# Kernel optimization log

Measured on AMD Instinct MI355X. Metric: run time of the kernel, lower is better.

## Reference

```python
import jax, jax.numpy as jnp
import numpy as np

B, N_NODE, E_PER, C, HID, HEADS, IN, NL = 16, 1024, 8192, 16, 128, 4, 32, 2
N = B * N_NODE
NEG_SLOPE = 0.2


def setup_inputs() -> dict:
    key = jax.random.key(0)
    ks = jax.random.split(key, 16)
    obs = jax.random.normal(ks[0], (N, IN), jnp.float32)
    # per-graph random edges, guaranteed no self-loops (GATv2Conv re-adds them once)
    src_l = jax.random.randint(ks[1], (B, E_PER), 0, N_NODE)
    off = jax.random.randint(ks[2], (B, E_PER), 1, N_NODE)
    dst_l = (src_l + off) % N_NODE
    base = (jnp.arange(B) * N_NODE)[:, None]
    edge_index = jnp.stack([(src_l + base).reshape(-1), (dst_l + base).reshape(-1)]).astype(jnp.int32)

    def lin(k, fi, fo):
        return (jax.random.normal(k, (fi, fo), jnp.float32) / np.sqrt(fi)).astype(jnp.float32)

    def gat(k):
        sk = jax.random.split(k, 3)
        return {
            'Wl': (jax.random.normal(sk[0], (NL, HID, HEADS * HID), jnp.float32) / np.sqrt(HID)),
            'bl': jnp.zeros((NL, HEADS * HID), jnp.float32),
            'Wr': (jax.random.normal(sk[1], (NL, HID, HEADS * HID), jnp.float32) / np.sqrt(HID)),
            'br': jnp.zeros((NL, HEADS * HID), jnp.float32),
            'att': (jax.random.normal(sk[2], (NL, HEADS, HID), jnp.float32) / np.sqrt(HID)),
            'bias': jnp.zeros((NL, HID), jnp.float32),
            'g': jnp.ones((NL, HID), jnp.float32),
            'beta': jnp.zeros((NL, HID), jnp.float32),
        }

    inp = {'obs': obs, 'edge_index': edge_index, 'n_node': N_NODE,
           'emb_W': lin(ks[3], IN, HID), 'emb_b': jnp.zeros((HID,), jnp.float32),
           'pool_W': lin(ks[4], HID, C), 'pool_b': jnp.zeros((C,), jnp.float32),
           'mlp_W1': lin(ks[5], HID, 4 * HID), 'mlp_b1': jnp.zeros((4 * HID,), jnp.float32),
           'mlp_W2': lin(ks[6], 4 * HID, HID), 'mlp_b2': jnp.zeros((HID,), jnp.float32)}
    for nm, d in (('low', gat(ks[7])), ('high', gat(ks[8]))):
        for k2, v in d.items():
            inp[nm + '_' + k2] = v
    return inp


def _layer_norm(x, g, b):
    mu = x.mean(-1, keepdims=True)
    v = jnp.mean((x - mu) ** 2, -1, keepdims=True)
    return (x - mu) / jnp.sqrt(v + 1e-5) * g + b


def _gatv2(x, src, dst, Wl, bl, Wr, br, att, bias):
    # GATv2Conv: heads H, concat=False (mean over heads), eval mode (no dropout)
    n = x.shape[0]
    H, D = att.shape
    xl = (x @ Wl + bl).reshape(n, H, D)  # source transform (lin_l)
    xr = (x @ Wr + br).reshape(n, H, D)  # target transform (lin_r)
    e = jax.nn.leaky_relu(xl[src] + xr[dst], NEG_SLOPE)  # [E,H,D]
    logit = jnp.einsum('ehd,hd->eh', e, att)
    m = jax.ops.segment_max(logit, dst, num_segments=n)
    p = jnp.exp(logit - m[dst])
    z = jax.ops.segment_sum(p, dst, num_segments=n)
    alpha = p / z[dst]
    out = jax.ops.segment_sum(alpha[:, :, None] * xl[src], dst, num_segments=n)
    return out.mean(axis=1) + bias


def _gat_stack(h, src, dst, Wl, bl, Wr, br, att, bias, g, beta):
    h_res = h
    nl = Wl.shape[0]
    for j in range(nl):
        h_in = h
        h = _gatv2(h, src, dst, Wl[j], bl[j], Wr[j], br[j], att[j], bias[j])
        h = _layer_norm(h, g[j], beta[j])
        if j != nl - 1:
            h = jax.nn.silu(h)
        h = h + h_in  # use_res=True
    return h + h_res


def _forward(obs, edge_index, n_node, emb_W, emb_b, pool_W, pool_b, mlp_W1, mlp_b1, mlp_W2, mlp_b2,
             low_Wl, low_bl, low_Wr, low_br, low_att, low_bias, low_g, low_beta,
             high_Wl, high_bl, high_Wr, high_br, high_att, high_bias, high_g, high_beta):
    n = obs.shape[0]
    h = obs @ emb_W + emb_b
    hh = h
    # low-level edges + self-loops (GATv2Conv add_self_loops; input has none)
    loops = jnp.arange(n, dtype=edge_index.dtype)
    src = jnp.concatenate([edge_index[0], loops])
    dst = jnp.concatenate([edge_index[1], loops])
    h = _gat_stack(h, src, dst, low_Wl, low_bl, low_Wr, low_br, low_att, low_bias, low_g, low_beta)
    # soft pooling
    pooling = jax.nn.softmax(h @ pool_W + pool_b, axis=-1)  # dim=1 == last dim on 2D
    b = n // n_node
    c = pooling.shape[-1]
    s = pooling.reshape(b, n_node, c)
    count = jnp.maximum(s.sum(axis=1), 1e-5)  # sT @ ones, clamp_min(1e-5)
    Hf = jnp.einsum('bnc,bnd->bcd', s, h.reshape(b, n_node, -1)) / count[:, :, None]
    Hf = Hf.reshape(b * c, -1)
    # high-level: fully connected per-graph cluster edges (self-loops already present once)
    hr = jnp.repeat(jnp.arange(c, dtype=jnp.int32), c)
    hc = jnp.tile(jnp.arange(c, dtype=jnp.int32), c)
    offb = (jnp.arange(b, dtype=jnp.int32) * c)[:, None]
    hsrc = (hr[None, :] + offb).reshape(-1)
    hdst = (hc[None, :] + offb).reshape(-1)
    Hf = _gat_stack(Hf, hsrc, hdst, high_Wl, high_bl, high_Wr, high_br, high_att, high_bias, high_g, high_beta)
    # unpool + residual MLP (BaseMLP flat=True: hidden=4*HID, Tanh, residual)
    l_H = jnp.einsum('bnc,bcd->bnd', s, Hf.reshape(b, c, -1)).reshape(n, -1)
    x = l_H + hh
    return jnp.tanh(x @ mlp_W1 + mlp_b1) @ mlp_W2 + mlp_b2 + x


def reference(obs, edge_index, n_node, emb_W, emb_b, pool_W, pool_b, mlp_W1, mlp_b1, mlp_W2, mlp_b2,
              low_Wl, low_bl, low_Wr, low_br, low_att, low_bias, low_g, low_beta,
              high_Wl, high_bl, high_Wr, high_br, high_att, high_bias, high_g, high_beta):
    return _forward(obs, edge_index, n_node, emb_W, emb_b, pool_W, pool_b, mlp_W1, mlp_b1, mlp_W2, mlp_b2,
                    low_Wl, low_bl, low_Wr, low_br, low_att, low_bias, low_g, low_beta,
                    high_Wl, high_bl, high_Wr, high_br, high_att, high_bias, high_g, high_beta)
```

## Files before the change

kernel.cpp:

```cpp
#include <hip/hip_runtime.h>
#include <math.h>

#define NTOT  16384
#define NNODE 1024

typedef unsigned short u16;
typedef unsigned short u16x8 __attribute__((ext_vector_type(8)));
typedef short s16x8 __attribute__((ext_vector_type(8)));
typedef float f32x4 __attribute__((ext_vector_type(4)));

static __device__ __forceinline__ float b2f(u16 u) {
  return __uint_as_float(((unsigned)u) << 16);
}
static __device__ __forceinline__ u16 f2b(float f) {
  unsigned x = __float_as_uint(f);
  return (u16)((x + 0x7FFFu + ((x >> 16) & 1u)) >> 16);
}

__global__ __launch_bounds__(64) void emb_k(const float* __restrict__ obs,
    const float* __restrict__ W, const float* __restrict__ b,
    float* __restrict__ h, float* __restrict__ hh, u16* __restrict__ h_bf)
{
  int n = blockIdx.x, l = threadIdx.x;
  __shared__ float ob[32];
  if (l < 32) ob[l] = obs[n * 32 + l];
  __syncthreads();
  float a0 = b[l], a1 = b[64 + l];
  #pragma unroll
  for (int k = 0; k < 32; ++k) {
    float o = ob[k];
    a0 = fmaf(o, W[k * 128 + l], a0);
    a1 = fmaf(o, W[k * 128 + 64 + l], a1);
  }
  size_t base = (size_t)n * 128;
  h[base + l] = a0;  h[base + 64 + l] = a1;
  hh[base + l] = a0; hh[base + 64 + l] = a1;
  h_bf[base + l] = f2b(a0); h_bf[base + 64 + l] = f2b(a1);
}

__global__ void hist_k(const int* __restrict__ ei, int E0, int* __restrict__ deg)
{
  int i = blockIdx.x * blockDim.x + threadIdx.x;
  int ET = E0 + NTOT;
  if (i < ET) {
    int d = (i < E0) ? ei[E0 + i] : (i - E0);
    atomicAdd(&deg[d], 1);
  }
}

__global__ __launch_bounds__(256) void scan_k(const int* __restrict__ deg,
    int* __restrict__ off, int* __restrict__ cursor)
{
  __shared__ int part[256];
  int t = threadIdx.x;
  int base = t * 64;
  int sum = 0;
  for (int i = 0; i < 64; ++i) sum += deg[base + i];
  part[t] = sum;
  __syncthreads();
  if (t == 0) {
    int run = 0;
    for (int i = 0; i < 256; ++i) { int v = part[i]; part[i] = run; run += v; }
  }
  __syncthreads();
  int run = part[t];
  for (int i = 0; i < 64; ++i) {
    off[base + i] = run; cursor[base + i] = run;
    run += deg[base + i];
  }
  if (t == 255) off[NTOT] = run;
}

__global__ void scat_k(const int* __restrict__ ei, int E0,
    int* __restrict__ cursor, int* __restrict__ csr_src)
{
  int i = blockIdx.x * blockDim.x + threadIdx.x;
  int ET = E0 + NTOT;
  if (i < ET) {
    int s, d;
    if (i < E0) { s = ei[i]; d = ei[E0 + i]; } else { s = d = i - E0; }
    int pos = atomicAdd(&cursor[d], 1);
    csr_src[pos] = s;
  }
}

__global__ void hi_k(int* __restrict__ hi_off, int* __restrict__ hi_src)
{
  int t = threadIdx.x;
  hi_off[t] = t * 16;
  if (t == 0) hi_off[256] = 4096;
  for (int i = t; i < 4096; i += 256) {
    int u = i >> 4;
    hi_src[i] = (u & ~15) + (i & 15);
  }
}

__global__ void wq_k(const float* __restrict__ W, u16* __restrict__ out,
                     int K, int N, int total)
{
  int idx = blockIdx.x * 256 + threadIdx.x;
  if (idx >= total) return;
  int kn = K * N;
  int m = idx / kn, r = idx - m * kn;
  int n = r / K, k = r - n * K;
  out[idx] = f2b(W[(size_t)m * kn + (size_t)k * N + n]);
}

__global__ __launch_bounds__(256) void gemm_bf16(
    const u16* __restrict__ A, const u16* __restrict__ Bt,
    const float* __restrict__ bias,
    float* __restrict__ Cf, u16* __restrict__ Cb,
    const float* __restrict__ res,
    int M, int K, int N, int act)
{
  __shared__ u16 Al[128][128];
  __shared__ u16 Bl[128][128];
  const int tid = threadIdx.x;
  const int bm = blockIdx.x * 128, bn = blockIdx.y * 128;
  const int w = tid >> 6, l = tid & 63;
  const int fr = l & 15;
  const int kg = l >> 4;
  const int sr = tid >> 1;
  const int sh = (tid & 1) << 3;

  f32x4 acc[2][8];
  #pragma unroll
  for (int a = 0; a < 2; ++a)
    #pragma unroll
    for (int b = 0; b < 8; ++b)
      acc[a][b] = (f32x4){0.f, 0.f, 0.f, 0.f};

  for (int k0 = 0; k0 < K; k0 += 128) {
    __syncthreads();
    const u16* As = A + (size_t)(bm + sr) * K + k0 + (sh << 3);
    const u16* Bs = Bt + (size_t)(bn + sr) * K + k0 + (sh << 3);
    #pragma unroll
    for (int i = 0; i < 8; ++i) {
      int gs = (sh + i) ^ (sr & 7);
      *(uint4*)&Al[sr][gs << 3] = *(const uint4*)(As + (i << 3));
    }
    #pragma unroll
    for (int i = 0; i < 8; ++i) {
      int gs = (sh + i) ^ (sr & 7);
      *(uint4*)&Bl[sr][gs << 3] = *(const uint4*)(Bs + (i << 3));
    }
    __syncthreads();
    #pragma unroll
    for (int ks = 0; ks < 4; ++ks) {
      const int g = (ks << 2) + kg;
      const int ar0 = w * 32 + fr, ar1 = ar0 + 16;
      s16x8 a0 = *(const s16x8*)&Al[ar0][(g ^ (ar0 & 7)) << 3];
      s16x8 a1 = *(const s16x8*)&Al[ar1][(g ^ (ar1 & 7)) << 3];
      #pragma unroll
      for (int nr = 0; nr < 8; ++nr) {
        const int br = nr * 16 + fr;
        s16x8 bb = *(const s16x8*)&Bl[br][(g ^ (br & 7)) << 3];
        acc[0][nr] = __builtin_amdgcn_mfma_f32_16x16x32_bf16(a0, bb, acc[0][nr], 0, 0, 0);
        acc[1][nr] = __builtin_amdgcn_mfma_f32_16x16x32_bf16(a1, bb, acc[1][nr], 0, 0, 0);
      }
    }
  }

  #pragma unroll
  for (int mr = 0; mr < 2; ++mr) {
    const int row0 = bm + w * 32 + mr * 16 + (kg << 2);
    #pragma unroll
    for (int nr = 0; nr < 8; ++nr) {
      const int col = bn + nr * 16 + fr;
      const float bb = bias[col];
      #pragma unroll
      for (int j = 0; j < 4; ++j) {
        float v = acc[mr][nr][j] + bb;
        if (act) v = tanhf(v);
        size_t o = (size_t)(row0 + j) * N + col;
        if (res) v += res[o];
        if (Cf) Cf[o] = v;
        if (Cb) Cb[o] = f2b(v);
      }
    }
  }
}

__global__ __launch_bounds__(64) void gat_agg(
    const u16* __restrict__ xl, const u16* __restrict__ xr,
    const int* __restrict__ off, const int* __restrict__ srcs,
    const float* __restrict__ att, const float* __restrict__ bias,
    const float* __restrict__ g, const float* __restrict__ beta,
    float* __restrict__ h, u16* __restrict__ h_bf,
    const float* __restrict__ res2, int do_silu, int swz)
{
  int b = blockIdx.x, l = threadIdx.x;
  int dst;
  if (swz) {
    int xcd = b & 7, i = b >> 3;
    dst = (((xcd << 1) + (i >> 10)) << 10) | (i & 1023);
  } else dst = b;

  float xrr[8], attr[8];
  {
    u16x8 vx = *(const u16x8*)(xr + (size_t)dst * 512 + l * 8);
    #pragma unroll
    for (int i = 0; i < 8; ++i) xrr[i] = b2f(vx[i]);
    const float4 a0 = *(const float4*)(att + l * 8);
    const float4 a1 = *(const float4*)(att + l * 8 + 4);
    attr[0] = a0.x; attr[1] = a0.y; attr[2] = a0.z; attr[3] = a0.w;
    attr[4] = a1.x; attr[5] = a1.y; attr[6] = a1.z; attr[7] = a1.w;
  }
  int e0 = off[dst], e1 = off[dst + 1];
  float m = -1e30f, z = 0.f;
  float acc[8] = {0.f, 0.f, 0.f, 0.f, 0.f, 0.f, 0.f, 0.f};
  int sB = (e0 + 1 < e1) ? srcs[e0 + 1] : 0;
  u16x8 vcur = *(const u16x8*)(xl + (size_t)srcs[e0] * 512 + l * 8);
  for (int e = e0; e < e1; ++e) {
    u16x8 vv = vcur;
    if (e + 1 < e1) {
      vcur = *(const u16x8*)(xl + (size_t)sB * 512 + l * 8);
      if (e + 2 < e1) sB = srcs[e + 2];
    }
    float xv[8];
    #pragma unroll
    for (int i = 0; i < 8; ++i) xv[i] = b2f(vv[i]);
    float part = 0.f;
    #pragma unroll
    for (int i = 0; i < 8; ++i) {
      float v = xv[i] + xrr[i];
      v = v > 0.f ? v : 0.2f * v;
      part = fmaf(v, attr[i], part);
    }
    part += __shfl_xor(part, 1); part += __shfl_xor(part, 2);
    part += __shfl_xor(part, 4); part += __shfl_xor(part, 8);
    float mn = fmaxf(m, part);
    float sc = __expf(m - mn);
    float p = __expf(part - mn);
    z = z * sc + p;
    #pragma unroll
    for (int i = 0; i < 8; ++i) acc[i] = fmaf(acc[i], sc, p * xv[i]);
    m = mn;
  }
  float inv = 0.25f / z;
  int d0 = (l & 15) * 8;
  float o[8];
  #pragma unroll
  for (int i = 0; i < 8; ++i) {
    float v = acc[i] * inv;
    v += __shfl_xor(v, 16);
    v += __shfl_xor(v, 32);
    o[i] = v + bias[d0 + i];
  }
  float ssum = 0.f;
  #pragma unroll
  for (int i = 0; i < 8; ++i) ssum += o[i];
  ssum += __shfl_xor(ssum, 1); ssum += __shfl_xor(ssum, 2);
  ssum += __shfl_xor(ssum, 4); ssum += __shfl_xor(ssum, 8);
  float mu = ssum * (1.f / 128.f);
  float vs = 0.f;
  #pragma unroll
  for (int i = 0; i < 8; ++i) { float d = o[i] - mu; vs += d * d; }
  vs += __shfl_xor(vs, 1); vs += __shfl_xor(vs, 2);
  vs += __shfl_xor(vs, 4); vs += __shfl_xor(vs, 8);
  float rstd = rsqrtf(vs * (1.f / 128.f) + 1e-5f);
  if (l < 16) {
    size_t base = (size_t)dst * 128 + d0;
    float out[8];
    u16x8 hb;
    #pragma unroll
    for (int i = 0; i < 8; ++i) {
      float y = (o[i] - mu) * rstd * g[d0 + i] + beta[d0 + i];
      if (do_silu) y = y / (1.f + __expf(-y));
      float r = h[base + i];
      if (res2) r += res2[base + i];
      out[i] = y + r;
      hb[i] = f2b(out[i]);
    }
    *(float4*)(h + base) = make_float4(out[0], out[1], out[2], out[3]);
    *(float4*)(h + base + 4) = make_float4(out[4], out[5], out[6], out[7]);
    *(u16x8*)(h_bf + base) = hb;
  }
}

__global__ __launch_bounds__(256) void pool_k(const float* __restrict__ h,
    const float* __restrict__ W, const float* __restrict__ b, float* __restrict__ s)
{
  __shared__ float hs[16 * 130];
  __shared__ float Ws[128 * 16];
  int t = threadIdx.x;
  int n0 = blockIdx.x * 16;
  #pragma unroll
  for (int i = 0; i < 8; ++i) {
    int idx = t + 256 * i;
    hs[(idx >> 7) * 130 + (idx & 127)] = h[(size_t)n0 * 128 + idx];
    Ws[idx] = W[idx];
  }
  __syncthreads();
  int nl = t >> 4, c = t & 15;
  float acc = b[c];
  for (int k = 0; k < 128; ++k) acc = fmaf(hs[nl * 130 + k], Ws[k * 16 + c], acc);
  float mx = acc;
  mx = fmaxf(mx, __shfl_xor(mx, 1)); mx = fmaxf(mx, __shfl_xor(mx, 2));
  mx = fmaxf(mx, __shfl_xor(mx, 4)); mx = fmaxf(mx, __shfl_xor(mx, 8));
  float p = __expf(acc - mx), sum = p;
  sum += __shfl_xor(sum, 1); sum += __shfl_xor(sum, 2);
  sum += __shfl_xor(sum, 4); sum += __shfl_xor(sum, 8);
  s[(size_t)(n0 + nl) * 16 + c] = p / sum;
}

#define HF_CHUNK 32
#define HF_NCH   32
__global__ __launch_bounds__(256) void hfp_k(const float* __restrict__ s,
    const float* __restrict__ h, float* __restrict__ part, float* __restrict__ cpart)
{
  __shared__ float ss[HF_CHUNK][16];
  __shared__ float hs[HF_CHUNK][128];
  int b = blockIdx.x >> 5, chunk = blockIdx.x & 31;
  int n0 = b * NNODE + chunk * HF_CHUNK;
  int t = threadIdx.x;
  if (t < 128) {
    float4 v = *(const float4*)(s + (size_t)(n0 + (t >> 2)) * 16 + (t & 3) * 4);
    *(float4*)&ss[t >> 2][(t & 3) * 4] = v;
  }
  #pragma unroll
  for (int i = 0; i < 4; ++i) {
    int idx = t + 256 * i;
    int row = idx >> 5, c4 = (idx & 31) * 4;
    *(float4*)&hs[row][c4] = *(const float4*)(h + (size_t)(n0 + row) * 128 + c4);
  }
  __syncthreads();
  int d = t & 127, cg = (t >> 7) * 8;
  float acc[8] = {};
  for (int n = 0; n < HF_CHUNK; ++n) {
    float hv = hs[n][d];
    #pragma unroll
    for (int i = 0; i < 8; ++i) acc[i] = fmaf(ss[n][cg + i], hv, acc[i]);
  }
  float* po = part + (size_t)chunk * 32768 + (size_t)(b * 16 + cg) * 128 + d;
  #pragma unroll
  for (int i = 0; i < 8; ++i) po[i * 128] = acc[i];
  if (t < 16) {
    float c = 0.f;
    #pragma unroll
    for (int n = 0; n < HF_CHUNK; ++n) c += ss[n][t];
    cpart[chunk * 256 + b * 16 + t] = c;
  }
}

__global__ __launch_bounds__(256) void hfr_k(const float* __restrict__ part,
    const float* __restrict__ cpart, float* __restrict__ Hf,
    float* __restrict__ HfRes, u16* __restrict__ Hf_bf)
{
  int o = blockIdx.x * 256 + threadIdx.x;
  int bc = o >> 7;
  float a = 0.f, cnt = 0.f;
  #pragma unroll 8
  for (int ch = 0; ch < HF_NCH; ++ch) {
    a += part[(size_t)ch * 32768 + o];
    cnt += cpart[ch * 256 + bc];
  }
  float v = a / fmaxf(cnt, 1e-5f);
  Hf[o] = v; HfRes[o] = v; Hf_bf[o] = f2b(v);
}

__global__ __launch_bounds__(64) void unpool_k(const float* __restrict__ s,
    const float* __restrict__ Hf, const float* __restrict__ hh,
    float* __restrict__ x, u16* __restrict__ x_bf)
{
  int n = blockIdx.x, l = threadIdx.x;
  int b = n >> 10;
  float a0 = 0.f, a1 = 0.f;
  #pragma unroll
  for (int c = 0; c < 16; ++c) {
    float sv = s[(size_t)n * 16 + c];
    const float* hp = Hf + (size_t)((b << 4) + c) * 128;
    a0 = fmaf(sv, hp[l], a0);
    a1 = fmaf(sv, hp[64 + l], a1);
  }
  size_t base = (size_t)n * 128;
  float v0 = a0 + hh[base + l], v1 = a1 + hh[base + 64 + l];
  x[base + l] = v0; x[base + 64 + l] = v1;
  x_bf[base + l] = f2b(v0); x_bf[base + 64 + l] = f2b(v1);
}

extern "C" void kernel_launch(void* const* d_in, const int* in_sizes, int n_in,
                              void* d_out, int out_size, void* d_ws, size_t ws_size,
                              hipStream_t stream) {
  (void)n_in; (void)out_size; (void)ws_size;
  const float* obs    = (const float*)d_in[0];
  const int*   ei     = (const int*)d_in[1];
  const float* emb_W  = (const float*)d_in[3];
  const float* emb_b  = (const float*)d_in[4];
  const float* pool_W = (const float*)d_in[5];
  const float* pool_b = (const float*)d_in[6];
  const float* mlp_W1 = (const float*)d_in[7];
  const float* mlp_b1 = (const float*)d_in[8];
  const float* mlp_W2 = (const float*)d_in[9];
  const float* mlp_b2 = (const float*)d_in[10];
  const float* lWl = (const float*)d_in[11]; const float* lbl = (const float*)d_in[12];
  const float* lWr = (const float*)d_in[13]; const float* lbr = (const float*)d_in[14];
  const float* latt = (const float*)d_in[15]; const float* lbias = (const float*)d_in[16];
  const float* lg = (const float*)d_in[17]; const float* lbeta = (const float*)d_in[18];
  const float* hWl = (const float*)d_in[19]; const float* hbl = (const float*)d_in[20];
  const float* hWr = (const float*)d_in[21]; const float* hbr = (const float*)d_in[22];
  const float* hatt = (const float*)d_in[23]; const float* hbias = (const float*)d_in[24];
  const float* hg = (const float*)d_in[25]; const float* hbeta = (const float*)d_in[26];

  const int E0 = in_sizes[1] / 2;
  const int ET = E0 + NTOT;

  char* p = (char*)d_ws;
  auto alloc = [&](size_t bytes) -> void* {
    void* q = (void*)p;
    p += (bytes + 255) & ~(size_t)255;
    return q;
  };
  float* h      = (float*)alloc((size_t)NTOT * 128 * 4);
  float* hh     = (float*)alloc((size_t)NTOT * 128 * 4);
  u16*   h_bf   = (u16*)alloc((size_t)NTOT * 128 * 2);
  u16*   xl_bf  = (u16*)alloc((size_t)NTOT * 512 * 2);
  u16*   xr_bf  = (u16*)alloc((size_t)NTOT * 512 * 2);
  u16*   x_bf   = (u16*)alloc((size_t)NTOT * 128 * 2);
  float* s      = (float*)alloc((size_t)NTOT * 16 * 4);
  float* Hf     = (float*)alloc(256 * 128 * 4);
  float* HfRes  = (float*)alloc(256 * 128 * 4);
  u16*   Hf_bf  = (u16*)alloc(256 * 128 * 2);
  u16*   hxl    = (u16*)alloc(256 * 512 * 2);
  u16*   hxr    = (u16*)alloc(256 * 512 * 2);
  float* hfPart = (float*)alloc((size_t)HF_NCH * 32768 * 4);
  float* hfCnt  = (float*)alloc((size_t)HF_NCH * 256 * 4);
  u16*   lWlT   = (u16*)alloc(2 * 512 * 128 * 2);
  u16*   lWrT   = (u16*)alloc(2 * 512 * 128 * 2);
  u16*   hWlT   = (u16*)alloc(2 * 512 * 128 * 2);
  u16*   hWrT   = (u16*)alloc(2 * 512 * 128 * 2);
  u16*   W1T    = (u16*)alloc(512 * 128 * 2);
  u16*   W2T    = (u16*)alloc(128 * 512 * 2);
  int* deg      = (int*)alloc((size_t)NTOT * 4);
  int* off      = (int*)alloc((size_t)(NTOT + 1) * 4);
  int* cursor   = (int*)alloc((size_t)NTOT * 4);
  int* csr      = (int*)alloc((size_t)ET * 4);
  int* hi_off   = (int*)alloc(257 * 4);
  int* hi_src   = (int*)alloc(4096 * 4);
  u16* t_bf     = xl_bf;

  wq_k<<<(2 * 65536 + 255) / 256, 256, 0, stream>>>(lWl, lWlT, 128, 512, 2 * 65536);
  wq_k<<<(2 * 65536 + 255) / 256, 256, 0, stream>>>(lWr, lWrT, 128, 512, 2 * 65536);
  wq_k<<<(2 * 65536 + 255) / 256, 256, 0, stream>>>(hWl, hWlT, 128, 512, 2 * 65536);
  wq_k<<<(2 * 65536 + 255) / 256, 256, 0, stream>>>(hWr, hWrT, 128, 512, 2 * 65536);
  wq_k<<<(65536 + 255) / 256, 256, 0, stream>>>(mlp_W1, W1T, 128, 512, 65536);
  wq_k<<<(65536 + 255) / 256, 256, 0, stream>>>(mlp_W2, W2T, 512, 128, 65536);

  hipMemsetAsync(deg, 0, (size_t)NTOT * 4, stream);
  emb_k<<<NTOT, 64, 0, stream>>>(obs, emb_W, emb_b, h, hh, h_bf);
  hist_k<<<(ET + 255) / 256, 256, 0, stream>>>(ei, E0, deg);
  scan_k<<<1, 256, 0, stream>>>(deg, off, cursor);
  scat_k<<<(ET + 255) / 256, 256, 0, stream>>>(ei, E0, cursor, csr);
  hi_k<<<1, 256, 0, stream>>>(hi_off, hi_src);

  for (int j = 0; j < 2; ++j) {
    gemm_bf16<<<dim3(NTOT / 128, 4), 256, 0, stream>>>(h_bf, lWlT + j * 65536,
        lbl + j * 512, nullptr, xl_bf, nullptr, NTOT, 128, 512, 0);
    gemm_bf16<<<dim3(NTOT / 128, 4), 256, 0, stream>>>(h_bf, lWrT + j * 65536,
        lbr + j * 512, nullptr, xr_bf, nullptr, NTOT, 128, 512, 0);
    gat_agg<<<NTOT, 64, 0, stream>>>(xl_bf, xr_bf, off, csr, latt + j * 512,
        lbias + j * 128, lg + j * 128, lbeta + j * 128, h, h_bf,
        j == 1 ? hh : nullptr, j == 0 ? 1 : 0, 1);
  }

  pool_k<<<NTOT / 16, 256, 0, stream>>>(h, pool_W, pool_b, s);
  hfp_k<<<16 * HF_NCH, 256, 0, stream>>>(s, h, hfPart, hfCnt);
  hfr_k<<<128, 256, 0, stream>>>(hfPart, hfCnt, Hf, HfRes, Hf_bf);

  for (int j = 0; j < 2; ++j) {
    gemm_bf16<<<dim3(2, 4), 256, 0, stream>>>(Hf_bf, hWlT + j * 65536,
        hbl + j * 512, nullptr, hxl, nullptr, 256, 128, 512, 0);
    gemm_bf16<<<dim3(2, 4), 256, 0, stream>>>(Hf_bf, hWrT + j * 65536,
        hbr + j * 512, nullptr, hxr, nullptr, 256, 128, 512, 0);
    gat_agg<<<256, 64, 0, stream>>>(hxl, hxr, hi_off, hi_src, hatt + j * 512,
        hbias + j * 128, hg + j * 128, hbeta + j * 128, Hf, Hf_bf,
        j == 1 ? HfRes : nullptr, j == 0 ? 1 : 0, 0);
  }

  float* x = (float*)d_out;
  unpool_k<<<NTOT, 64, 0, stream>>>(s, Hf, hh, x, x_bf);
  gemm_bf16<<<dim3(NTOT / 128, 4), 256, 0, stream>>>(x_bf, W1T, mlp_b1,
      nullptr, t_bf, nullptr, NTOT, 128, 512, 1);
  gemm_bf16<<<dim3(NTOT / 128, 1), 256, 0, stream>>>(t_bf, W2T, mlp_b2,
      x, nullptr, x, NTOT, 512, 128, 0);
}
```

Before: 421.1 us.

## Fuse Wl/Wr projection GEMMs and process two destination nodes per GAT block

The left and right projection weights are concatenated into one transposed bf16 matrix, so a single GEMM with a split epilogue writes xl and xr and halves the number of GEMM launches. The aggregation kernel now handles two destination nodes per 64-thread block, interleaving their edge loops so the gathers for both nodes can overlap. Loop iterations past a node's degree are masked out. The gains are fewer launches, better latency hiding and coalesced float4 residual reads, at the cost of extra registers and wasted work when the two nodes have very different degrees.

```diff
diff --git a/kernel.cpp b/kernel.cpp
--- a/kernel.cpp
+++ b/kernel.cpp
@@ -106,12 +106,24 @@
   out[idx] = f2b(W[(size_t)m * kn + (size_t)k * N + n]);
 }
 
+__global__ void wq2_k(const float* __restrict__ Wl, const float* __restrict__ Wr,
+                      u16* __restrict__ out, int total)
+{
+  int idx = blockIdx.x * 256 + threadIdx.x;
+  if (idx >= total) return;
+  int m = idx >> 17;
+  int r = idx & 131071;
+  int n = r >> 7, k = r & 127;
+  const float* W = (n < 512) ? Wl : Wr;
+  out[idx] = f2b(W[(size_t)m * 65536 + (size_t)k * 512 + (n & 511)]);
+}
+
 __global__ __launch_bounds__(256) void gemm_bf16(
     const u16* __restrict__ A, const u16* __restrict__ Bt,
-    const float* __restrict__ bias,
-    float* __restrict__ Cf, u16* __restrict__ Cb,
+    const float* __restrict__ bias0, const float* __restrict__ bias1,
+    float* __restrict__ Cf, u16* __restrict__ Cb0, u16* __restrict__ Cb1,
     const float* __restrict__ res,
-    int M, int K, int N, int act)
+    int M, int K, int N, int Nsplit, int act)
 {
   __shared__ u16 Al[128][128];
   __shared__ u16 Bl[128][128];
@@ -167,21 +179,50 @@
     #pragma unroll
     for (int nr = 0; nr < 8; ++nr) {
       const int col = bn + nr * 16 + fr;
-      const float bb = bias[col];
+      const int half = (col >= Nsplit);
+      const int c2 = half ? col - Nsplit : col;
+      const int str = half ? (N - Nsplit) : Nsplit;
+      const float bb = half ? bias1[c2] : bias0[c2];
+      u16* cb = half ? Cb1 : Cb0;
       #pragma unroll
       for (int j = 0; j < 4; ++j) {
         float v = acc[mr][nr][j] + bb;
         if (act) v = tanhf(v);
-        size_t o = (size_t)(row0 + j) * N + col;
+        size_t o = (size_t)(row0 + j) * str + c2;
         if (res) v += res[o];
         if (Cf) Cf[o] = v;
-        if (Cb) Cb[o] = f2b(v);
+        if (cb) cb[o] = f2b(v);
       }
     }
   }
 }
 
-__global__ __launch_bounds__(64) void gat_agg(
+static __device__ __forceinline__ void edge_step(
+    u16x8 vv, bool valid, const float* xrr, const float* attr,
+    float& m, float& z, float* acc)
+{
+  float xv[8];
+  #pragma unroll
+  for (int i = 0; i < 8; ++i) xv[i] = b2f(vv[i]);
+  float part = 0.f;
+  #pragma unroll
+  for (int i = 0; i < 8; ++i) {
+    float v = xv[i] + xrr[i];
+    part = fmaf(fmaxf(v, 0.2f * v), attr[i], part);
+  }
+  part += __shfl_xor(part, 1); part += __shfl_xor(part, 2);
+  part += __shfl_xor(part, 4); part += __shfl_xor(part, 8);
+  if (!valid) part = -1e30f;
+  float mn = fmaxf(m, part);
+  float sc = __expf(m - mn);
+  float p  = __expf(part - mn);
+  z = z * sc + p;
+  #pragma unroll
+  for (int i = 0; i < 8; ++i) acc[i] = fmaf(acc[i], sc, p * xv[i]);
+  m = mn;
+}
+
+__global__ __launch_bounds__(64) void gat_agg2(
     const u16* __restrict__ xl, const u16* __restrict__ xr,
     const int* __restrict__ off, const int* __restrict__ srcs,
     const float* __restrict__ att, const float* __restrict__ bias,
@@ -190,86 +231,106 @@
     const float* __restrict__ res2, int do_silu, int swz)
 {
   int b = blockIdx.x, l = threadIdx.x;
-  int dst;
+  int dst0;
   if (swz) {
     int xcd = b & 7, i = b >> 3;
-    dst = (((xcd << 1) + (i >> 10)) << 10) | (i & 1023);
-  } else dst = b;
-
-  float xrr[8], attr[8];
+    dst0 = (((xcd << 1) + (i >> 9)) << 10) | ((i & 511) << 1);
+  } else dst0 = b << 1;
+  const int dst1 = dst0 + 1;
+
+  float attr[8];
   {
-    u16x8 vx = *(const u16x8*)(xr + (size_t)dst * 512 + l * 8);
-    #pragma unroll
-    for (int i = 0; i < 8; ++i) xrr[i] = b2f(vx[i]);
     const float4 a0 = *(const float4*)(att + l * 8);
     const float4 a1 = *(const float4*)(att + l * 8 + 4);
     attr[0] = a0.x; attr[1] = a0.y; attr[2] = a0.z; attr[3] = a0.w;
     attr[4] = a1.x; attr[5] = a1.y; attr[6] = a1.z; attr[7] = a1.w;
   }
-  int e0 = off[dst], e1 = off[dst + 1];
-  float m = -1e30f, z = 0.f;
-  float acc[8] = {0.f, 0.f, 0.f, 0.f, 0.f, 0.f, 0.f, 0.f};
-  int sB = (e0 + 1 < e1) ? srcs[e0 + 1] : 0;
-  u16x8 vcur = *(const u16x8*)(xl + (size_t)srcs[e0] * 512 + l * 8);
-  for (int e = e0; e < e1; ++e) {
-    u16x8 vv = vcur;
-    if (e + 1 < e1) {
-      vcur = *(const u16x8*)(xl + (size_t)sB * 512 + l * 8);
-      if (e + 2 < e1) sB = srcs[e + 2];
-    }
-    float xv[8];
-    #pragma unroll
-    for (int i = 0; i < 8; ++i) xv[i] = b2f(vv[i]);
-    float part = 0.f;
-    #pragma unroll
-    for (int i = 0; i < 8; ++i) {
-      float v = xv[i] + xrr[i];
-      v = v > 0.f ? v : 0.2f * v;
-      part = fmaf(v, attr[i], part);
-    }
-    part += __shfl_xor(part, 1); part += __shfl_xor(part, 2);
-    part += __shfl_xor(part, 4); part += __shfl_xor(part, 8);
-    float mn = fmaxf(m, part);
-    float sc = __expf(m - mn);
-    float p = __expf(part - mn);
-    z = z * sc + p;
-    #pragma unroll
-    for (int i = 0; i < 8; ++i) acc[i] = fmaf(acc[i], sc, p * xv[i]);
-    m = mn;
-  }
-  float inv = 0.25f / z;
-  int d0 = (l & 15) * 8;
-  float o[8];
+  float xrr0[8], xrr1[8];
+  {
+    u16x8 v0 = *(const u16x8*)(xr + (size_t)dst0 * 512 + l * 8);
+    u16x8 v1 = *(const u16x8*)(xr + (size_t)dst1 * 512 + l * 8);
+    #pragma unroll
+    for (int i = 0; i < 8; ++i) { xrr0[i] = b2f(v0[i]); xrr1[i] = b2f(v1[i]); }
+  }
+  const int s0 = off[dst0], n0 = off[dst0 + 1] - s0;
+  const int s1 = off[dst1], n1 = off[dst1 + 1] - s1;
+  const int nmax = n0 > n1 ? n0 : n1;
+
+  int ni0 = (n0 > 1) ? srcs[s0 + 1] : 0;
+  int ni1 = (n1 > 1) ? srcs[s1 + 1] : 0;
+  u16x8 v0 = *(const u16x8*)(xl + (size_t)srcs[s0] * 512 + l * 8);
+  u16x8 v1 = *(const u16x8*)(xl + (size_t)srcs[s1] * 512 + l * 8);
+
+  float m0 = -1e30f, z0 = 0.f, acc0[8] = {};
+  float m1 = -1e30f, z1 = 0.f, acc1[8] = {};
+
+  for (int e = 0; e < nmax; ++e) {
+    u16x8 c0 = v0, c1 = v1;
+    if (e + 1 < nmax) {
+      v0 = *(const u16x8*)(xl + (size_t)ni0 * 512 + l * 8);
+      v1 = *(const u16x8*)(xl + (size_t)ni1 * 512 + l * 8);
+      if (e + 2 < n0) ni0 = srcs[s0 + e + 2];
+      if (e + 2 < n1) ni1 = srcs[s1 + e + 2];
+    }
+    edge_step(c0, e < n0, xrr0, attr, m0, z0, acc0);
+    edge_step(c1, e < n1, xrr1, attr, m1, z1, acc1);
+  }
+
+  const int d0 = (l & 15) * 8;
+  float o0[8], o1[8];
+  const float inv0 = 0.25f / z0, inv1 = 0.25f / z1;
   #pragma unroll
   for (int i = 0; i < 8; ++i) {
-    float v = acc[i] * inv;
-    v += __shfl_xor(v, 16);
-    v += __shfl_xor(v, 32);
-    o[i] = v + bias[d0 + i];
-  }
-  float ssum = 0.f;
-  #pragma unroll
-  for (int i = 0; i < 8; ++i) ssum += o[i];
-  ssum += __shfl_xor(ssum, 1); ssum += __shfl_xor(ssum, 2);
-  ssum += __shfl_xor(ssum, 4); ssum += __shfl_xor(ssum, 8);
-  float mu = ssum * (1.f / 128.f);
-  float vs = 0.f;
-  #pragma unroll
-  for (int i = 0; i < 8; ++i) { float d = o[i] - mu; vs += d * d; }
-  vs += __shfl_xor(vs, 1); vs += __shfl_xor(vs, 2);
-  vs += __shfl_xor(vs, 4); vs += __shfl_xor(vs, 8);
-  float rstd = rsqrtf(vs * (1.f / 128.f) + 1e-5f);
-  if (l < 16) {
-    size_t base = (size_t)dst * 128 + d0;
+    float v = acc0[i] * inv0;
+    v += __shfl_xor(v, 16); v += __shfl_xor(v, 32);
+    o0[i] = v + bias[d0 + i];
+    float w2 = acc1[i] * inv1;
+    w2 += __shfl_xor(w2, 16); w2 += __shfl_xor(w2, 32);
+    o1[i] = w2 + bias[d0 + i];
+  }
+  float sa = 0.f, sb = 0.f;
+  #pragma unroll
+  for (int i = 0; i < 8; ++i) { sa += o0[i]; sb += o1[i]; }
+  sa += __shfl_xor(sa, 1); sa += __shfl_xor(sa, 2);
+  sa += __shfl_xor(sa, 4); sa += __shfl_xor(sa, 8);
+  sb += __shfl_xor(sb, 1); sb += __shfl_xor(sb, 2);
+  sb += __shfl_xor(sb, 4); sb += __shfl_xor(sb, 8);
+  const float mu0 = sa * (1.f / 128.f), mu1 = sb * (1.f / 128.f);
+  float va = 0.f, vb = 0.f;
+  #pragma unroll
+  for (int i = 0; i < 8; ++i) {
+    float d = o0[i] - mu0; va += d * d;
+    float e = o1[i] - mu1; vb += e * e;
+  }
+  va += __shfl_xor(va, 1); va += __shfl_xor(va, 2);
+  va += __shfl_xor(va, 4); va += __shfl_xor(va, 8);
+  vb += __shfl_xor(vb, 1); vb += __shfl_xor(vb, 2);
+  vb += __shfl_xor(vb, 4); vb += __shfl_xor(vb, 8);
+  const float rstd0 = rsqrtf(va * (1.f / 128.f) + 1e-5f);
+  const float rstd1 = rsqrtf(vb * (1.f / 128.f) + 1e-5f);
+
+  const float* oo = (l < 16) ? o0 : o1;
+  const float mu = (l < 16) ? mu0 : mu1;
+  const float rstd = (l < 16) ? rstd0 : rstd1;
+  const int dd = (l < 16) ? dst0 : dst1;
+  if (l < 32) {
+    size_t base = (size_t)dd * 128 + d0;
+    float4 r0 = *(const float4*)(h + base);
+    float4 r1 = *(const float4*)(h + base + 4);
+    float rr[8] = {r0.x, r0.y, r0.z, r0.w, r1.x, r1.y, r1.z, r1.w};
+    if (res2) {
+      float4 q0 = *(const float4*)(res2 + base);
+      float4 q1 = *(const float4*)(res2 + base + 4);
+      rr[0] += q0.x; rr[1] += q0.y; rr[2] += q0.z; rr[3] += q0.w;
+      rr[4] += q1.x; rr[5] += q1.y; rr[6] += q1.z; rr[7] += q1.w;
+    }
     float out[8];
     u16x8 hb;
     #pragma unroll
     for (int i = 0; i < 8; ++i) {
-      float y = (o[i] - mu) * rstd * g[d0 + i] + beta[d0 + i];
+      float y = (oo[i] - mu) * rstd * g[d0 + i] + beta[d0 + i];
       if (do_silu) y = y / (1.f + __expf(-y));
-      float r = h[base + i];
-      if (res2) r += res2[base + i];
-      out[i] = y + r;
+      out[i] = y + rr[i];
       hb[i] = f2b(out[i]);
     }
     *(float4*)(h + base) = make_float4(out[0], out[1], out[2], out[3]);
@@ -425,10 +486,8 @@
   u16*   hxr    = (u16*)alloc(256 * 512 * 2);
   float* hfPart = (float*)alloc((size_t)HF_NCH * 32768 * 4);
   float* hfCnt  = (float*)alloc((size_t)HF_NCH * 256 * 4);
-  u16*   lWlT   = (u16*)alloc(2 * 512 * 128 * 2);
-  u16*   lWrT   = (u16*)alloc(2 * 512 * 128 * 2);
-  u16*   hWlT   = (u16*)alloc(2 * 512 * 128 * 2);
-  u16*   hWrT   = (u16*)alloc(2 * 512 * 128 * 2);
+  u16*   lWT    = (u16*)alloc(2 * 1024 * 128 * 2);
+  u16*   hWT    = (u16*)alloc(2 * 1024 * 128 * 2);
   u16*   W1T    = (u16*)alloc(512 * 128 * 2);
   u16*   W2T    = (u16*)alloc(128 * 512 * 2);
   int* deg      = (int*)alloc((size_t)NTOT * 4);
@@ -439,10 +498,8 @@
   int* hi_src   = (int*)alloc(4096 * 4);
   u16* t_bf     = xl_bf;
 
-  wq_k<<<(2 * 65536 + 255) / 256, 256, 0, stream>>>(lWl, lWlT, 128, 512, 2 * 65536);
-  wq_k<<<(2 * 65536 + 255) / 256, 256, 0, stream>>>(lWr, lWrT, 128, 512, 2 * 65536);
-  wq_k<<<(2 * 65536 + 255) / 256, 256, 0, stream>>>(hWl, hWlT, 128, 512, 2 * 65536);
-  wq_k<<<(2 * 65536 + 255) / 256, 256, 0, stream>>>(hWr, hWrT, 128, 512, 2 * 65536);
+  wq2_k<<<(2 * 131072 + 255) / 256, 256, 0, stream>>>(lWl, lWr, lWT, 2 * 131072);
+  wq2_k<<<(2 * 131072 + 255) / 256, 256, 0, stream>>>(hWl, hWr, hWT, 2 * 131072);
   wq_k<<<(65536 + 255) / 256, 256, 0, stream>>>(mlp_W1, W1T, 128, 512, 65536);
   wq_k<<<(65536 + 255) / 256, 256, 0, stream>>>(mlp_W2, W2T, 512, 128, 65536);
 
@@ -454,11 +511,10 @@
   hi_k<<<1, 256, 0, stream>>>(hi_off, hi_src);
 
   for (int j = 0; j < 2; ++j) {
-    gemm_bf16<<<dim3(NTOT / 128, 4), 256, 0, stream>>>(h_bf, lWlT + j * 65536,
-        lbl + j * 512, nullptr, xl_bf, nullptr, NTOT, 128, 512, 0);
-    gemm_bf16<<<dim3(NTOT / 128, 4), 256, 0, stream>>>(h_bf, lWrT + j * 65536,
-        lbr + j * 512, nullptr, xr_bf, nullptr, NTOT, 128, 512, 0);
-    gat_agg<<<NTOT, 64, 0, stream>>>(xl_bf, xr_bf, off, csr, latt + j * 512,
+    gemm_bf16<<<dim3(NTOT / 128, 8), 256, 0, stream>>>(h_bf, lWT + j * 131072,
+        lbl + j * 512, lbr + j * 512, nullptr, xl_bf, xr_bf, nullptr,
+        NTOT, 128, 1024, 512, 0);
+    gat_agg2<<<NTOT / 2, 64, 0, stream>>>(xl_bf, xr_bf, off, csr, latt + j * 512,
         lbias + j * 128, lg + j * 128, lbeta + j * 128, h, h_bf,
         j == 1 ? hh : nullptr, j == 0 ? 1 : 0, 1);
   }
@@ -468,19 +524,18 @@
   hfr_k<<<128, 256, 0, stream>>>(hfPart, hfCnt, Hf, HfRes, Hf_bf);
 
   for (int j = 0; j < 2; ++j) {
-    gemm_bf16<<<dim3(2, 4), 256, 0, stream>>>(Hf_bf, hWlT + j * 65536,
-        hbl + j * 512, nullptr, hxl, nullptr, 256, 128, 512, 0);
-    gemm_bf16<<<dim3(2, 4), 256, 0, stream>>>(Hf_bf, hWrT + j * 65536,
-        hbr + j * 512, nullptr, hxr, nullptr, 256, 128, 512, 0);
-    gat_agg<<<256, 64, 0, stream>>>(hxl, hxr, hi_off, hi_src, hatt + j * 512,
+    gemm_bf16<<<dim3(2, 8), 256, 0, stream>>>(Hf_bf, hWT + j * 131072,
+        hbl + j * 512, hbr + j * 512, nullptr, hxl, hxr, nullptr,
+        256, 128, 1024, 512, 0);
+    gat_agg2<<<128, 64, 0, stream>>>(hxl, hxr, hi_off, hi_src, hatt + j * 512,
         hbias + j * 128, hg + j * 128, hbeta + j * 128, Hf, Hf_bf,
         j == 1 ? HfRes : nullptr, j == 0 ? 1 : 0, 0);
   }
 
   float* x = (float*)d_out;
   unpool_k<<<NTOT, 64, 0, stream>>>(s, Hf, hh, x, x_bf);
-  gemm_bf16<<<dim3(NTOT / 128, 4), 256, 0, stream>>>(x_bf, W1T, mlp_b1,
-      nullptr, t_bf, nullptr, NTOT, 128, 512, 1);
-  gemm_bf16<<<dim3(NTOT / 128, 1), 256, 0, stream>>>(t_bf, W2T, mlp_b2,
-      x, nullptr, x, NTOT, 512, 128, 0);
-}
+  gemm_bf16<<<dim3(NTOT / 128, 4), 256, 0, stream>>>(x_bf, W1T, mlp_b1, nullptr,
+      nullptr, t_bf, nullptr, nullptr, NTOT, 128, 512, 512, 1);
+  gemm_bf16<<<dim3(NTOT / 128, 1), 256, 0, stream>>>(t_bf, W2T, mlp_b2, nullptr,
+      x, nullptr, nullptr, x, NTOT, 512, 128, 128, 0);
+}
```

Result: faster. 398.6 us (-5.4%).
